# Optimization experiments

Measured on AMD Instinct MI355X. Metric: run time of the kernel, lower is better.

Reference implementation:

```python
import jax, jax.numpy as jnp
import numpy as np

EPS = 1e-8
NUM_ITERATIONS = 3


def layer_norm(x, g, b, eps=EPS):
    m = jnp.mean(x, axis=-1, keepdims=True)
    v = jnp.mean((x - m) ** 2, axis=-1, keepdims=True)
    return (x - m) * jax.lax.rsqrt(v + eps) * g + b


def gru_cell(x, h, w_ih, w_hh, b_ih, b_hh):
    # PyTorch GRUCell: gates ordered (r, z, n)
    gi = x @ w_ih.T + b_ih  # [B*S, 3D]
    gh = h @ w_hh.T + b_hh
    i_r, i_z, i_n = jnp.split(gi, 3, axis=-1)
    h_r, h_z, h_n = jnp.split(gh, 3, axis=-1)
    r = jax.nn.sigmoid(i_r + h_r)
    z = jax.nn.sigmoid(i_z + h_z)
    n = jnp.tanh(i_n + r * h_n)
    return (1.0 - z) * n + z * h


def setup_inputs() -> dict:
    key = jax.random.key(0)
    ks = jax.random.split(key, 12)
    B, N, D, S = 64, 1024, 512, 16
    s = 1.0 / np.sqrt(D)
    return {
        "inputs": jax.random.normal(ks[0], (B, N, D), jnp.float32),
        "noise": jax.random.normal(ks[1], (B, S, D), jnp.float32),
        "slot_mu": jax.random.normal(ks[2], (1, 1, D), jnp.float32),
        "slot_log_sigma": jnp.zeros((1, 1, D), jnp.float32),
        "ln_in_g": jnp.ones((D,), jnp.float32),
        "ln_in_b": jnp.zeros((D,), jnp.float32),
        "ln_slots_g": jnp.ones((D,), jnp.float32),
        "ln_slots_b": jnp.zeros((D,), jnp.float32),
        "ln_mlp_g": jnp.ones((D,), jnp.float32),
        "ln_mlp_b": jnp.zeros((D,), jnp.float32),
        "Wq": jax.random.normal(ks[3], (D, D), jnp.float32) * s,
        "Wk": jax.random.normal(ks[4], (D, D), jnp.float32) * s,
        "Wv": jax.random.normal(ks[5], (D, D), jnp.float32) * s,
        "gru_w_ih": jax.random.normal(ks[6], (3 * D, D), jnp.float32) * s,
        "gru_w_hh": jax.random.normal(ks[7], (3 * D, D), jnp.float32) * s,
        "gru_b_ih": jnp.zeros((3 * D,), jnp.float32),
        "gru_b_hh": jnp.zeros((3 * D,), jnp.float32),
        "mlp_w1": jax.random.normal(ks[8], (D, D), jnp.float32) * s,
        "mlp_b1": jnp.zeros((D,), jnp.float32),
        "mlp_w2": jax.random.normal(ks[9], (D, D), jnp.float32) * s,
        "mlp_b2": jnp.zeros((D,), jnp.float32),
    }


def reference(inputs, noise, slot_mu, slot_log_sigma,
              ln_in_g, ln_in_b, ln_slots_g, ln_slots_b, ln_mlp_g, ln_mlp_b,
              Wq, Wk, Wv, gru_w_ih, gru_w_hh, gru_b_ih, gru_b_hh,
              mlp_w1, mlp_b1, mlp_w2, mlp_b2):
    B, N, D = inputs.shape
    S = noise.shape[1]
    scale = D ** (-0.5)

    # slot init: mu + sigma * eps
    slots = slot_mu + jnp.exp(slot_log_sigma) * noise  # [B,S,D]

    x = layer_norm(inputs, ln_in_g, ln_in_b)
    k = x @ Wk.T  # [B,N,D]
    v = x @ Wv.T

    for _ in range(NUM_ITERATIONS):
        slots_prev = slots
        sn = layer_norm(slots, ln_slots_g, ln_slots_b)
        q = sn @ Wq.T  # [B,S,D]
        attn_logits = jnp.einsum("bnd,bmd->bnm", q, k) * scale  # [B,S,N]
        attn = jax.nn.softmax(attn_logits, axis=-1)
        attn = attn / (jnp.sum(attn, axis=1, keepdims=True) + EPS)  # column-normalize over slots
        updates = jnp.einsum("bnm,bmd->bnd", attn, v)  # [B,S,D]
        slots = gru_cell(updates.reshape(-1, D), slots_prev.reshape(-1, D),
                         gru_w_ih, gru_w_hh, gru_b_ih, gru_b_hh).reshape(B, S, D)
        h = jax.nn.relu(layer_norm(slots, ln_mlp_g, ln_mlp_b) @ mlp_w1.T + mlp_b1)
        slots = slots + h @ mlp_w2.T + mlp_b2

    # proj_to_hidden is Identity (slot_dim == hidden_size); forward_dtype=float32
    return slots
```

## Files before the change

### kernel.cpp

```cpp
#include <hip/hip_runtime.h>
#include <hip/hip_bf16.h>
#include <cstdint>
#include <cstddef>


typedef __bf16 bf16x8 __attribute__((ext_vector_type(8)));
typedef float f32x4 __attribute__((ext_vector_type(4)));

__device__ __forceinline__ float bf2f(unsigned int u) {
  union { unsigned int i; float f; } v; v.i = u << 16; return v.f;
}
__device__ __forceinline__ unsigned short f2bf(float x) {
  __hip_bfloat16 h = __float2bfloat16(x);
  unsigned short u;
  __builtin_memcpy(&u, &h, 2);
  return u;
}

#define GLD16(gp, lp)                                                       \
  __builtin_amdgcn_global_load_lds(                                         \
      (const __attribute__((address_space(1))) void*)(gp),                  \
      (__attribute__((address_space(3))) void*)(lp), 16, 0, 0)


__global__ void cast_bf16_k(const float* __restrict__ in, unsigned short* __restrict__ out, int n) {
  int i = blockIdx.x * 256 + threadIdx.x;
  if (i < n) out[i] = f2bf(in[i]);
}

__global__ __launch_bounds__(256) void tcast_k(const float* __restrict__ in,
                                               unsigned short* __restrict__ out) {
  __shared__ float t[32][33];
  int c0 = blockIdx.x << 5, r0 = blockIdx.y << 5;
  int tx = threadIdx.x & 31, ty = threadIdx.x >> 5;
  #pragma unroll
  for (int i = 0; i < 4; ++i)
    t[ty + 8 * i][tx] = in[(size_t)(r0 + ty + 8 * i) * 512 + c0 + tx];
  __syncthreads();
  #pragma unroll
  for (int i = 0; i < 4; ++i)
    out[(size_t)(c0 + ty + 8 * i) * 512 + r0 + tx] = f2bf(t[tx][ty + 8 * i]);
}

__global__ void init_slots_k(const float* __restrict__ mu, const float* __restrict__ ls,
                             const float* __restrict__ noise, float* __restrict__ slots) {
  int i = blockIdx.x * 256 + threadIdx.x;
  int d = i & 511;
  slots[i] = mu[d] + expf(ls[d]) * noise[i];
}

__global__ void wcat_k(const float* __restrict__ wih, const float* __restrict__ whh,
                       unsigned short* __restrict__ out) {
  int i = blockIdx.x * 256 + threadIdx.x;
  int j = i >> 10, k = i & 1023;
  float v;
  if (j < 1024)      v = (k < 512) ? wih[j * 512 + k] : whh[j * 512 + (k - 512)];
  else if (j < 1536) v = (k < 512) ? wih[j * 512 + k] : 0.0f;
  else               v = (k < 512) ? 0.0f : whh[(j - 512) * 512 + (k - 512)];
  out[i] = f2bf(v);
}

__global__ void bcat_k(const float* __restrict__ bih, const float* __restrict__ bhh,
                       float* __restrict__ out) {
  int j = blockIdx.x * 256 + threadIdx.x;
  float v;
  if (j < 1024)      v = bih[j] + bhh[j];
  else if (j < 1536) v = bih[j];
  else               v = bhh[j - 512];
  out[j] = v;
}


__global__ __launch_bounds__(256) void ln_rows_k(
    const float* __restrict__ in, const float* __restrict__ g, const float* __restrict__ b,
    unsigned short* __restrict__ out, int rows) {
  int w = threadIdx.x >> 6, lane = threadIdx.x & 63;
  int row = (blockIdx.x << 2) + w;
  if (row >= rows) return;
  const float4* rp = reinterpret_cast<const float4*>(in + (size_t)row * 512);
  float4 v0 = rp[lane], v1 = rp[lane + 64];
  float s = v0.x + v0.y + v0.z + v0.w + v1.x + v1.y + v1.z + v1.w;
  float q = v0.x*v0.x + v0.y*v0.y + v0.z*v0.z + v0.w*v0.w
          + v1.x*v1.x + v1.y*v1.y + v1.z*v1.z + v1.w*v1.w;
  #pragma unroll
  for (int o = 32; o > 0; o >>= 1) { s += __shfl_xor(s, o); q += __shfl_xor(q, o); }
  float m = s * (1.0f / 512.0f);
  float rstd = rsqrtf(q * (1.0f / 512.0f) - m * m + 1e-8f);
  const float4* gp = reinterpret_cast<const float4*>(g);
  const float4* bp = reinterpret_cast<const float4*>(b);
  float4 g0 = gp[lane], g1 = gp[lane + 64];
  float4 b0 = bp[lane], b1 = bp[lane + 64];
  ushort4 o0, o1;
  o0.x = f2bf((v0.x - m) * rstd * g0.x + b0.x);
  o0.y = f2bf((v0.y - m) * rstd * g0.y + b0.y);
  o0.z = f2bf((v0.z - m) * rstd * g0.z + b0.z);
  o0.w = f2bf((v0.w - m) * rstd * g0.w + b0.w);
  o1.x = f2bf((v1.x - m) * rstd * g1.x + b1.x);
  o1.y = f2bf((v1.y - m) * rstd * g1.y + b1.y);
  o1.z = f2bf((v1.z - m) * rstd * g1.z + b1.z);
  o1.w = f2bf((v1.w - m) * rstd * g1.w + b1.w);
  ushort4* op = reinterpret_cast<ushort4*>(out + (size_t)row * 512);
  op[lane] = o0; op[lane + 64] = o1;
}

__global__ __launch_bounds__(256) void ln_cast_k(
    const float* __restrict__ in, const float* __restrict__ g, const float* __restrict__ b,
    unsigned short* __restrict__ sn, unsigned short* __restrict__ A2) {
  int w = threadIdx.x >> 6, lane = threadIdx.x & 63;
  int row = (blockIdx.x << 2) + w;
  const float4* rp = reinterpret_cast<const float4*>(in + (size_t)row * 512);
  float4 v0 = rp[lane], v1 = rp[lane + 64];
  float s = v0.x + v0.y + v0.z + v0.w + v1.x + v1.y + v1.z + v1.w;
  float q = v0.x*v0.x + v0.y*v0.y + v0.z*v0.z + v0.w*v0.w
          + v1.x*v1.x + v1.y*v1.y + v1.z*v1.z + v1.w*v1.w;
  #pragma unroll
  for (int o = 32; o > 0; o >>= 1) { s += __shfl_xor(s, o); q += __shfl_xor(q, o); }
  float m = s * (1.0f / 512.0f);
  float rstd = rsqrtf(q * (1.0f / 512.0f) - m * m + 1e-8f);
  const float4* gp = reinterpret_cast<const float4*>(g);
  const float4* bp = reinterpret_cast<const float4*>(b);
  float4 g0 = gp[lane], g1 = gp[lane + 64];
  float4 b0 = bp[lane], b1 = bp[lane + 64];
  ushort4 c0, c1, o0, o1;
  c0.x = f2bf(v0.x); c0.y = f2bf(v0.y); c0.z = f2bf(v0.z); c0.w = f2bf(v0.w);
  c1.x = f2bf(v1.x); c1.y = f2bf(v1.y); c1.z = f2bf(v1.z); c1.w = f2bf(v1.w);
  o0.x = f2bf((v0.x - m) * rstd * g0.x + b0.x);
  o0.y = f2bf((v0.y - m) * rstd * g0.y + b0.y);
  o0.z = f2bf((v0.z - m) * rstd * g0.z + b0.z);
  o0.w = f2bf((v0.w - m) * rstd * g0.w + b0.w);
  o1.x = f2bf((v1.x - m) * rstd * g1.x + b1.x);
  o1.y = f2bf((v1.y - m) * rstd * g1.y + b1.y);
  o1.z = f2bf((v1.z - m) * rstd * g1.z + b1.z);
  o1.w = f2bf((v1.w - m) * rstd * g1.w + b1.w);
  ushort4* sp_ = reinterpret_cast<ushort4*>(sn + (size_t)row * 512);
  ushort4* cp_ = reinterpret_cast<ushort4*>(A2 + (size_t)row * 1024 + 512);
  sp_[lane] = o0; sp_[lane + 64] = o1;
  cp_[lane] = c0; cp_[lane + 64] = c1;
}

__global__ __launch_bounds__(256) void gru_ln_k(
    const float* __restrict__ gates, const float* __restrict__ hp,
    const float* __restrict__ g, const float* __restrict__ b,
    float* __restrict__ sgru, unsigned short* __restrict__ lnm) {
  int w = threadIdx.x >> 6, lane = threadIdx.x & 63;
  int row = (blockIdx.x << 2) + w;
  size_t gb = (size_t)row * 2048 + (lane << 3);
  size_t hb = (size_t)row * 512 + (lane << 3);
  float rs[8], zs[8], in_[8], hn[8], hv[8], y[8];
  #pragma unroll
  for (int c = 0; c < 2; ++c) {
    *reinterpret_cast<float4*>(rs + 4*c)  = *reinterpret_cast<const float4*>(gates + gb + 4*c);
    *reinterpret_cast<float4*>(zs + 4*c)  = *reinterpret_cast<const float4*>(gates + gb + 512 + 4*c);
    *reinterpret_cast<float4*>(in_ + 4*c) = *reinterpret_cast<const float4*>(gates + gb + 1024 + 4*c);
    *reinterpret_cast<float4*>(hn + 4*c)  = *reinterpret_cast<const float4*>(gates + gb + 1536 + 4*c);
    *reinterpret_cast<float4*>(hv + 4*c)  = *reinterpret_cast<const float4*>(hp + hb + 4*c);
  }
  float s = 0.f, q = 0.f;
  #pragma unroll
  for (int j = 0; j < 8; ++j) {
    float r = 1.0f / (1.0f + expf(-rs[j]));
    float z = 1.0f / (1.0f + expf(-zs[j]));
    float n = tanhf(in_[j] + r * hn[j]);
    float h = (1.0f - z) * n + z * hv[j];
    y[j] = h; s += h; q += h * h;
  }
  #pragma unroll
  for (int o = 32; o > 0; o >>= 1) { s += __shfl_xor(s, o); q += __shfl_xor(q, o); }
  float m = s * (1.0f / 512.0f);
  float rstd = rsqrtf(q * (1.0f / 512.0f) - m * m + 1e-8f);
  const float* gg = g + (lane << 3);
  const float* bb = b + (lane << 3);
  #pragma unroll
  for (int c = 0; c < 2; ++c)
    *reinterpret_cast<float4*>(sgru + hb + 4*c) = *reinterpret_cast<const float4*>(y + 4*c);
  uint4 o4;
  unsigned int p[8];
  #pragma unroll
  for (int j = 0; j < 8; ++j) p[j] = f2bf((y[j] - m) * rstd * gg[j] + bb[j]);
  o4.x = p[0] | (p[1] << 16); o4.y = p[2] | (p[3] << 16);
  o4.z = p[4] | (p[5] << 16); o4.w = p[6] | (p[7] << 16);
  *reinterpret_cast<uint4*>(lnm + hb) = o4;
}


__global__ __launch_bounds__(256) void gemm_vt(
    const unsigned short* __restrict__ A, const unsigned short* __restrict__ W,
    unsigned short* __restrict__ vT) {
  __shared__ unsigned short sA[2][4096];
  __shared__ unsigned short sB[2][4096];
  const int tid = threadIdx.x;
  const int lane = tid & 63, w = tid >> 6;

  int flat = blockIdx.y * 4 + blockIdx.x;
  { int c = 2048 >> 3; flat = (flat & 7) * c + (flat >> 3); }
  const int row0 = (flat >> 2) << 7;
  const int col0 = (flat & 3) << 7;
  const int K = 512;

  const int wm = (w >> 1) << 6, wn = (w & 1) << 6;
  const int lrow = lane & 15, kt = (lane >> 4) << 3;
  const int srow = lane >> 2, scol = (lane & 3) << 3;

  f32x4 acc[4][4];
  #pragma unroll
  for (int m = 0; m < 4; ++m)
    #pragma unroll
    for (int n = 0; n < 4; ++n) acc[m][n] = f32x4{0.f, 0.f, 0.f, 0.f};

  auto stage = [&](int buf, int k0) {
    #pragma unroll
    for (int i = 0; i < 2; ++i) {
      int ii = w * 2 + i;
      int r = (ii << 4) + srow;
      GLD16(A + (size_t)(row0 + r) * K + k0 + scol, &sA[buf][ii * 512]);
      GLD16(W + (size_t)(col0 + r) * K + k0 + scol, &sB[buf][ii * 512]);
    }
  };

  stage(0, 0);
  int cur = 0;
  for (int t = 0; t < 16; ++t) {
    __syncthreads();
    if (t + 1 < 16) stage(cur ^ 1, (t + 1) << 5);
    bf16x8 af[4], bfv[4];
    #pragma unroll
    for (int m = 0; m < 4; ++m)
      af[m] = *reinterpret_cast<const bf16x8*>(&sA[cur][(wm + m * 16 + lrow) * 32 + kt]);
    #pragma unroll
    for (int n = 0; n < 4; ++n)
      bfv[n] = *reinterpret_cast<const bf16x8*>(&sB[cur][(wn + n * 16 + lrow) * 32 + kt]);
    #pragma unroll
    for (int m = 0; m < 4; ++m)
      #pragma unroll
      for (int n = 0; n < 4; ++n)
        acc[m][n] = __builtin_amdgcn_mfma_f32_16x16x32_bf16(af[m], bfv[n], acc[m][n], 0, 0, 0);
    cur ^= 1;
  }

  const int rb = (lane >> 4) << 2;
  const int b = row0 >> 10;
  const int n0 = row0 & 1023;
  unsigned short* vb = vT + ((size_t)b << 19);
  #pragma unroll
  for (int m = 0; m < 4; ++m) {
    #pragma unroll
    for (int n = 0; n < 4; ++n) {
      int col = col0 + wn + n * 16 + lrow;
      int nn = n0 + wm + m * 16 + rb;
      ushort4 o;
      o.x = f2bf(acc[m][n][0]); o.y = f2bf(acc[m][n][1]);
      o.z = f2bf(acc[m][n][2]); o.w = f2bf(acc[m][n][3]);
      *reinterpret_cast<ushort4*>(vb + (size_t)col * 1024 + nn) = o;
    }
  }
}


__global__ __launch_bounds__(256) void q2_k(
    const unsigned short* __restrict__ sn, const unsigned short* __restrict__ wpt,
    unsigned short* __restrict__ q2) {
  __shared__ unsigned short sA[2][512];
  __shared__ unsigned short sB[2][4096];
  const int b = blockIdx.y, ct = blockIdx.x;
  const int lane = threadIdx.x & 63, w = threadIdx.x >> 6;
  const int lrow = lane & 15, kt = (lane >> 4) << 3;
  const int srow = lane >> 2, scol = (lane & 3) << 3;
  const unsigned short* Ab = sn + ((size_t)b << 13);
  const unsigned short* Bb = wpt + (size_t)(ct << 7) * 512;

  f32x4 acc[2];
  acc[0] = f32x4{0.f, 0.f, 0.f, 0.f};
  acc[1] = f32x4{0.f, 0.f, 0.f, 0.f};

  auto stage = [&](int buf, int k0) {
    #pragma unroll
    for (int i = 0; i < 2; ++i) {
      int ii = w * 2 + i;
      GLD16(Bb + (size_t)((ii << 4) + srow) * 512 + k0 + scol, &sB[buf][ii * 512]);
    }
    if (w == 0)
      GLD16(Ab + (size_t)srow * 512 + k0 + scol, &sA[buf][0]);
  };

  stage(0, 0);
  int cur = 0;
  for (int t = 0; t < 16; ++t) {
    __syncthreads();
    if (t + 1 < 16) stage(cur ^ 1, (t + 1) << 5);
    bf16x8 af = *reinterpret_cast<const bf16x8*>(&sA[cur][lrow * 32 + kt]);
    #pragma unroll
    for (int ni = 0; ni < 2; ++ni) {
      bf16x8 bfv = *reinterpret_cast<const bf16x8*>(&sB[cur][((w * 2 + ni) * 16 + lrow) * 32 + kt]);
      acc[ni] = __builtin_amdgcn_mfma_f32_16x16x32_bf16(af, bfv, acc[ni], 0, 0, 0);
    }
    cur ^= 1;
  }

  const int rb = (lane >> 4) << 2;
  #pragma unroll
  for (int ni = 0; ni < 2; ++ni) {
    int col = (ct << 7) + (w * 2 + ni) * 16 + lrow;
    #pragma unroll
    for (int r = 0; r < 4; ++r) {
      int s = rb + r;
      q2[(size_t)((b << 4) + s) * 512 + col] = f2bf(acc[ni][r]);
    }
  }
}


__global__ __launch_bounds__(256) void logits_k(
    const unsigned short* __restrict__ q2, const unsigned short* __restrict__ x,
    float* __restrict__ out) {
  __shared__ unsigned short sA[2][512];
  __shared__ unsigned short sB[2][4096];
  const int b = blockIdx.y, nt = blockIdx.x;
  const int lane = threadIdx.x & 63, w = threadIdx.x >> 6;
  const int lrow = lane & 15, kt = (lane >> 4) << 3;
  const int srow = lane >> 2, scol = (lane & 3) << 3;
  const unsigned short* Ab = q2 + ((size_t)b << 13);
  const unsigned short* Bb = x + (((size_t)(b << 10) + (nt << 7)) << 9);

  f32x4 acc[2];
  acc[0] = f32x4{0.f, 0.f, 0.f, 0.f};
  acc[1] = f32x4{0.f, 0.f, 0.f, 0.f};

  auto stage = [&](int buf, int k0) {
    #pragma unroll
    for (int i = 0; i < 2; ++i) {
      int ii = w * 2 + i;
      GLD16(Bb + (size_t)((ii << 4) + srow) * 512 + k0 + scol, &sB[buf][ii * 512]);
    }
    if (w == 0)
      GLD16(Ab + (size_t)srow * 512 + k0 + scol, &sA[buf][0]);
  };

  stage(0, 0);
  int cur = 0;
  for (int t = 0; t < 16; ++t) {
    __syncthreads();
    if (t + 1 < 16) stage(cur ^ 1, (t + 1) << 5);
    bf16x8 af = *reinterpret_cast<const bf16x8*>(&sA[cur][lrow * 32 + kt]);
    #pragma unroll
    for (int ni = 0; ni < 2; ++ni) {
      bf16x8 bfv = *reinterpret_cast<const bf16x8*>(&sB[cur][((w * 2 + ni) * 16 + lrow) * 32 + kt]);
      acc[ni] = __builtin_amdgcn_mfma_f32_16x16x32_bf16(af, bfv, acc[ni], 0, 0, 0);
    }
    cur ^= 1;
  }

  const int rb = (lane >> 4) << 2;
  #pragma unroll
  for (int ni = 0; ni < 2; ++ni) {
    int n = (nt << 7) + (w * 2 + ni) * 16 + lrow;
    #pragma unroll
    for (int r = 0; r < 4; ++r) {
      int s = rb + r;
      out[(size_t)((b << 4) + s) * 1024 + n] = acc[ni][r];
    }
  }
}


__global__ __launch_bounds__(1024) void softmax_cn_k(
    const float* __restrict__ logits, unsigned short* __restrict__ attn) {
  __shared__ float sp[16][1024];
  int b = blockIdx.x;
  int w = threadIdx.x >> 6, lane = threadIdx.x & 63;
  const float* rp = logits + ((size_t)b * 16 + w) * 1024;
  float v[16];
  float mx = -3.4e38f;
  #pragma unroll
  for (int i = 0; i < 16; ++i) { v[i] = rp[lane + (i << 6)]; mx = fmaxf(mx, v[i]); }
  #pragma unroll
  for (int o = 32; o > 0; o >>= 1) mx = fmaxf(mx, __shfl_xor(mx, o));
  float s = 0.f;
  #pragma unroll
  for (int i = 0; i < 16; ++i) { v[i] = __expf(v[i] - mx); s += v[i]; }
  #pragma unroll
  for (int o = 32; o > 0; o >>= 1) s += __shfl_xor(s, o);
  float inv = 1.0f / s;
  #pragma unroll
  for (int i = 0; i < 16; ++i) sp[w][lane + (i << 6)] = v[i] * inv;
  __syncthreads();
  int col = threadIdx.x;
  float cs = 0.f;
  #pragma unroll
  for (int s2 = 0; s2 < 16; ++s2) cs += sp[s2][col];
  float rinv = 1.0f / (cs + 1e-8f);
  unsigned short* ob = attn + ((size_t)b << 14);
  #pragma unroll
  for (int s2 = 0; s2 < 16; ++s2) ob[s2 * 1024 + col] = f2bf(sp[s2][col] * rinv);
}


__global__ __launch_bounds__(256) void pv_k(
    const unsigned short* __restrict__ vT, const unsigned short* __restrict__ attn,
    unsigned short* __restrict__ A2) {
  __shared__ unsigned short sA[2][4096];
  __shared__ unsigned short sB[2][512];
  const int b = blockIdx.y, dt = blockIdx.x;
  const int lane = threadIdx.x & 63, w = threadIdx.x >> 6;
  const int lrow = lane & 15, kt = (lane >> 4) << 3;
  const int srow = lane >> 2, scol = (lane & 3) << 3;
  const unsigned short* Ab = vT + ((size_t)b << 19) + (size_t)(dt << 7) * 1024;
  const unsigned short* Bb = attn + ((size_t)b << 14);

  f32x4 acc[2];
  acc[0] = f32x4{0.f, 0.f, 0.f, 0.f};
  acc[1] = f32x4{0.f, 0.f, 0.f, 0.f};

  auto stage = [&](int buf, int k0) {
    #pragma unroll
    for (int i = 0; i < 2; ++i) {
      int ii = w * 2 + i;
      GLD16(Ab + (size_t)((ii << 4) + srow) * 1024 + k0 + scol, &sA[buf][ii * 512]);
    }
    if (w == 0)
      GLD16(Bb + (size_t)srow * 1024 + k0 + scol, &sB[buf][0]);
  };

  stage(0, 0);
  int cur = 0;
  for (int t = 0; t < 32; ++t) {
    __syncthreads();
    if (t + 1 < 32) stage(cur ^ 1, (t + 1) << 5);
    bf16x8 bfv = *reinterpret_cast<const bf16x8*>(&sB[cur][lrow * 32 + kt]);
    #pragma unroll
    for (int mi = 0; mi < 2; ++mi) {
      bf16x8 af = *reinterpret_cast<const bf16x8*>(&sA[cur][((w * 2 + mi) * 16 + lrow) * 32 + kt]);
      acc[mi] = __builtin_amdgcn_mfma_f32_16x16x32_bf16(af, bfv, acc[mi], 0, 0, 0);
    }
    cur ^= 1;
  }

  const int rb = (lane >> 4) << 2;
  const int s = lrow;
  #pragma unroll
  for (int mi = 0; mi < 2; ++mi) {
    int d0 = (dt << 7) + (w * 2 + mi) * 16 + rb;
    ushort4 o;
    o.x = f2bf(acc[mi][0]); o.y = f2bf(acc[mi][1]);
    o.z = f2bf(acc[mi][2]); o.w = f2bf(acc[mi][3]);
    *reinterpret_cast<ushort4*>(&A2[(size_t)((b << 4) + s) * 1024 + d0]) = o;
  }
}


template<int BIAS, int RELU, int ADDSRC, int OUTBF16, int SCALE>
__global__ __launch_bounds__(256) void gemm_sm(
    const unsigned short* __restrict__ A, const unsigned short* __restrict__ W,
    const float* __restrict__ bias, const float* __restrict__ addsrc,
    void* __restrict__ Cout, int M, int N, int K, float scalev) {
  __shared__ unsigned short sA[2][2048];
  __shared__ unsigned short sB[2][2048];
  const int tid = threadIdx.x;
  const int lane = tid & 63, w = tid >> 6;

  int nwg = gridDim.x * gridDim.y;
  int flat = blockIdx.y * gridDim.x + blockIdx.x;
  if ((nwg & 7) == 0) { int c = nwg >> 3; flat = (flat & 7) * c + (flat >> 3); }
  const int row0 = (flat / gridDim.x) << 6;
  const int col0 = (flat % gridDim.x) << 6;

  const int lrow = lane & 15, kt = (lane >> 4) << 3;
  const int srow = lane >> 2, scol = (lane & 3) << 3;

  f32x4 acc[4];
  #pragma unroll
  for (int m = 0; m < 4; ++m) acc[m] = f32x4{0.f, 0.f, 0.f, 0.f};

  auto stage = [&](int buf, int k0) {
    int r = (w << 4) + srow;
    GLD16(A + (size_t)(row0 + r) * K + k0 + scol, &sA[buf][w * 512]);
    GLD16(W + (size_t)(col0 + r) * K + k0 + scol, &sB[buf][w * 512]);
  };

  stage(0, 0);
  const int nt = K >> 5;
  int cur = 0;
  for (int t = 0; t < nt; ++t) {
    __syncthreads();
    if (t + 1 < nt) stage(cur ^ 1, (t + 1) << 5);
    bf16x8 af[4], bfv;
    #pragma unroll
    for (int m = 0; m < 4; ++m)
      af[m] = *reinterpret_cast<const bf16x8*>(&sA[cur][(m * 16 + lrow) * 32 + kt]);
    bfv = *reinterpret_cast<const bf16x8*>(&sB[cur][((w << 4) + lrow) * 32 + kt]);
    #pragma unroll
    for (int m = 0; m < 4; ++m)
      acc[m] = __builtin_amdgcn_mfma_f32_16x16x32_bf16(af[m], bfv, acc[m], 0, 0, 0);
    cur ^= 1;
  }

  const int rb = (lane >> 4) << 2;
  const int col = col0 + (w << 4) + lrow;
  float bv = BIAS ? bias[col] : 0.0f;
  #pragma unroll
  for (int m = 0; m < 4; ++m) {
    #pragma unroll
    for (int r = 0; r < 4; ++r) {
      int row = row0 + m * 16 + rb + r;
      float v = acc[m][r];
      if (SCALE) v *= scalev;
      v += bv;
      if (ADDSRC) v += addsrc[(size_t)row * N + col];
      if (RELU) v = fmaxf(v, 0.0f);
      if (OUTBF16) ((unsigned short*)Cout)[(size_t)row * N + col] = f2bf(v);
      else ((float*)Cout)[(size_t)row * N + col] = v;
    }
  }
}


extern "C" void kernel_launch(void* const* d_in, const int* in_sizes, int n_in,
                              void* d_out, int out_size, void* d_ws, size_t ws_size,
                              hipStream_t stream) {
  const float* inputs  = (const float*)d_in[0];
  const float* noise   = (const float*)d_in[1];
  const float* slot_mu = (const float*)d_in[2];
  const float* slot_ls = (const float*)d_in[3];
  const float* ln_in_g = (const float*)d_in[4];
  const float* ln_in_b = (const float*)d_in[5];
  const float* ln_s_g  = (const float*)d_in[6];
  const float* ln_s_b  = (const float*)d_in[7];
  const float* ln_m_g  = (const float*)d_in[8];
  const float* ln_m_b  = (const float*)d_in[9];
  const float* Wq   = (const float*)d_in[10];
  const float* Wk   = (const float*)d_in[11];
  const float* Wv   = (const float*)d_in[12];
  const float* w_ih = (const float*)d_in[13];
  const float* w_hh = (const float*)d_in[14];
  const float* b_ih = (const float*)d_in[15];
  const float* b_hh = (const float*)d_in[16];
  const float* w1   = (const float*)d_in[17];
  const float* b1   = (const float*)d_in[18];
  const float* w2   = (const float*)d_in[19];
  const float* b2   = (const float*)d_in[20];

  const int BN = 65536, BS = 1024;

  uintptr_t base = (uintptr_t)d_ws;
  auto alloc = [&](size_t bytes) {
    void* p = (void*)base;
    base += (bytes + 255) & ~(size_t)255;
    return p;
  };
  unsigned short* x_bf    = (unsigned short*)alloc((size_t)BN * 512 * 2);
  unsigned short* vT      = (unsigned short*)alloc((size_t)64 * 512 * 1024 * 2);
  unsigned short* wqT     = (unsigned short*)alloc(512 * 512 * 2);
  unsigned short* wkT     = (unsigned short*)alloc(512 * 512 * 2);
  unsigned short* wpt     = (unsigned short*)alloc(512 * 512 * 2);
  unsigned short* wv_bf   = (unsigned short*)alloc(512 * 512 * 2);
  unsigned short* wcat_bf = (unsigned short*)alloc((size_t)2048 * 1024 * 2);
  float*          bcat    = (float*)alloc(2048 * 4);
  unsigned short* w1_bf   = (unsigned short*)alloc(512 * 512 * 2);
  unsigned short* w2_bf   = (unsigned short*)alloc(512 * 512 * 2);
  float*          slots   = (float*)alloc((size_t)BS * 512 * 4);
  unsigned short* sn_bf   = (unsigned short*)alloc((size_t)BS * 512 * 2);
  unsigned short* A2      = (unsigned short*)alloc((size_t)BS * 1024 * 2);
  unsigned short* q2_bf   = (unsigned short*)alloc((size_t)BS * 512 * 2);
  float*          logits  = (float*)alloc((size_t)64 * 16 * 1024 * 4);
  unsigned short* attn_bf = (unsigned short*)alloc((size_t)64 * 16 * 1024 * 2);
  float*          gates   = (float*)alloc((size_t)BS * 2048 * 4);
  float*          sgru    = (float*)alloc((size_t)BS * 512 * 4);
  unsigned short* lnm_bf  = (unsigned short*)alloc((size_t)BS * 512 * 2);
  unsigned short* h_bf    = (unsigned short*)alloc((size_t)BS * 512 * 2);
  (void)ws_size; (void)n_in; (void)in_sizes; (void)out_size;

  const float scale = 0.044194173824159216f;

  tcast_k<<<dim3(16, 16), 256, 0, stream>>>(Wq, wqT);
  tcast_k<<<dim3(16, 16), 256, 0, stream>>>(Wk, wkT);
  gemm_sm<0,0,0,1,1><<<dim3(8, 8), 256, 0, stream>>>(
      wkT, wqT, nullptr, nullptr, wpt, 512, 512, 512, scale);
  cast_bf16_k<<<1024, 256, 0, stream>>>(Wv, wv_bf, 262144);
  wcat_k<<<8192, 256, 0, stream>>>(w_ih, w_hh, wcat_bf);
  bcat_k<<<8, 256, 0, stream>>>(b_ih, b_hh, bcat);
  cast_bf16_k<<<1024, 256, 0, stream>>>(w1, w1_bf, 262144);
  cast_bf16_k<<<1024, 256, 0, stream>>>(w2, w2_bf, 262144);

  init_slots_k<<<2048, 256, 0, stream>>>(slot_mu, slot_ls, noise, slots);
  ln_rows_k<<<16384, 256, 0, stream>>>(inputs, ln_in_g, ln_in_b, x_bf, BN);
  gemm_vt<<<dim3(4, 512), 256, 0, stream>>>(x_bf, wv_bf, vT);

  for (int it = 0; it < 3; ++it) {
    ln_cast_k<<<256, 256, 0, stream>>>(slots, ln_s_g, ln_s_b, sn_bf, A2);
    q2_k<<<dim3(4, 64), 256, 0, stream>>>(sn_bf, wpt, q2_bf);
    logits_k<<<dim3(8, 64), 256, 0, stream>>>(q2_bf, x_bf, logits);
    softmax_cn_k<<<64, 1024, 0, stream>>>(logits, attn_bf);
    pv_k<<<dim3(4, 64), 256, 0, stream>>>(vT, attn_bf, A2);
    gemm_sm<1,0,0,0,0><<<dim3(32, 16), 256, 0, stream>>>(
        A2, wcat_bf, bcat, nullptr, gates, BS, 2048, 1024, 1.0f);
    gru_ln_k<<<256, 256, 0, stream>>>(gates, slots, ln_m_g, ln_m_b, sgru, lnm_bf);
    gemm_sm<1,1,0,1,0><<<dim3(8, 16), 256, 0, stream>>>(
        lnm_bf, w1_bf, b1, nullptr, h_bf, BS, 512, 512, 1.0f);
    float* slots_out = (it == 2) ? (float*)d_out : slots;
    gemm_sm<1,0,1,0,0><<<dim3(8, 16), 256, 0, stream>>>(
        h_bf, w2_bf, b2, sgru, slots_out, BS, 512, 512, 1.0f);
  }
}
```

Baseline: 365.9 us.

## Fuse slot layernorm into Q GEMM, softmax into PV, and merge setup kernels

Merges the weight cast, concat, bias and slot-init setup kernels into a single launch, and the two transpose-casts into one. In each iteration the slot layernorm moves into the Q-projection kernel and the softmax plus column normalisation moves into the PV kernel, which drops the intermediate sn and attn buffers and several launches. The cost is redundant work: each of the four column tiles recomputes the layernorm and the full softmax for its batch, and extra shared memory is used per block.

Result: no change. 368.9 us (+0.8%).

```diff
diff --git a/kernel.cpp b/kernel.cpp
--- a/kernel.cpp
+++ b/kernel.cpp
@@ -23,51 +23,59 @@
       (__attribute__((address_space(3))) void*)(lp), 16, 0, 0)
 
 
-__global__ void cast_bf16_k(const float* __restrict__ in, unsigned short* __restrict__ out, int n) {
-  int i = blockIdx.x * 256 + threadIdx.x;
-  if (i < n) out[i] = f2bf(in[i]);
-}
-
-__global__ __launch_bounds__(256) void tcast_k(const float* __restrict__ in,
-                                               unsigned short* __restrict__ out) {
-  __shared__ float t[32][33];
+__global__ void wprep_k(const float* __restrict__ Wv, const float* __restrict__ w1,
+                        const float* __restrict__ w2, const float* __restrict__ wih,
+                        const float* __restrict__ whh, const float* __restrict__ bih,
+                        const float* __restrict__ bhh, const float* __restrict__ mu,
+                        const float* __restrict__ ls, const float* __restrict__ noise,
+                        unsigned short* __restrict__ wv_bf, unsigned short* __restrict__ w1_bf,
+                        unsigned short* __restrict__ w2_bf, unsigned short* __restrict__ wcat,
+                        float* __restrict__ bcat, float* __restrict__ slots) {
+  int blk = blockIdx.x, t = threadIdx.x;
+  if (blk < 1024) {
+    int i = blk * 256 + t; wv_bf[i] = f2bf(Wv[i]);
+  } else if (blk < 2048) {
+    int i = (blk - 1024) * 256 + t; w1_bf[i] = f2bf(w1[i]);
+  } else if (blk < 3072) {
+    int i = (blk - 2048) * 256 + t; w2_bf[i] = f2bf(w2[i]);
+  } else if (blk < 11264) {
+    int i = (blk - 3072) * 256 + t;
+    int j = i >> 10, k = i & 1023;
+    float v;
+    if (j < 1024)      v = (k < 512) ? wih[j * 512 + k] : whh[j * 512 + (k - 512)];
+    else if (j < 1536) v = (k < 512) ? wih[j * 512 + k] : 0.0f;
+    else               v = (k < 512) ? 0.0f : whh[(j - 512) * 512 + (k - 512)];
+    wcat[i] = f2bf(v);
+  } else if (blk < 11272) {
+    int j = (blk - 11264) * 256 + t;
+    float v;
+    if (j < 1024)      v = bih[j] + bhh[j];
+    else if (j < 1536) v = bih[j];
+    else               v = bhh[j - 512];
+    bcat[j] = v;
+  } else {
+    int i = (blk - 11272) * 256 + t;
+    int d = i & 511;
+    slots[i] = mu[d] + expf(ls[d]) * noise[i];
+  }
+}
+
+__global__ __launch_bounds__(256) void tcast2_k(const float* __restrict__ Wq,
+                                                const float* __restrict__ Wk,
+                                                unsigned short* __restrict__ wqT,
+                                                unsigned short* __restrict__ wkT) {
+  __shared__ float tt[32][33];
+  const float* in = blockIdx.z ? Wk : Wq;
+  unsigned short* out = blockIdx.z ? wkT : wqT;
   int c0 = blockIdx.x << 5, r0 = blockIdx.y << 5;
   int tx = threadIdx.x & 31, ty = threadIdx.x >> 5;
   #pragma unroll
   for (int i = 0; i < 4; ++i)
-    t[ty + 8 * i][tx] = in[(size_t)(r0 + ty + 8 * i) * 512 + c0 + tx];
+    tt[ty + 8 * i][tx] = in[(size_t)(r0 + ty + 8 * i) * 512 + c0 + tx];
   __syncthreads();
   #pragma unroll
   for (int i = 0; i < 4; ++i)
-    out[(size_t)(c0 + ty + 8 * i) * 512 + r0 + tx] = f2bf(t[tx][ty + 8 * i]);
-}
-
-__global__ void init_slots_k(const float* __restrict__ mu, const float* __restrict__ ls,
-                             const float* __restrict__ noise, float* __restrict__ slots) {
-  int i = blockIdx.x * 256 + threadIdx.x;
-  int d = i & 511;
-  slots[i] = mu[d] + expf(ls[d]) * noise[i];
-}
-
-__global__ void wcat_k(const float* __restrict__ wih, const float* __restrict__ whh,
-                       unsigned short* __restrict__ out) {
-  int i = blockIdx.x * 256 + threadIdx.x;
-  int j = i >> 10, k = i & 1023;
-  float v;
-  if (j < 1024)      v = (k < 512) ? wih[j * 512 + k] : whh[j * 512 + (k - 512)];
-  else if (j < 1536) v = (k < 512) ? wih[j * 512 + k] : 0.0f;
-  else               v = (k < 512) ? 0.0f : whh[(j - 512) * 512 + (k - 512)];
-  out[i] = f2bf(v);
-}
-
-__global__ void bcat_k(const float* __restrict__ bih, const float* __restrict__ bhh,
-                       float* __restrict__ out) {
-  int j = blockIdx.x * 256 + threadIdx.x;
-  float v;
-  if (j < 1024)      v = bih[j] + bhh[j];
-  else if (j < 1536) v = bih[j];
-  else               v = bhh[j - 512];
-  out[j] = v;
+    out[(size_t)(c0 + ty + 8 * i) * 512 + r0 + tx] = f2bf(tt[tx][ty + 8 * i]);
 }
 
 
@@ -103,41 +111,6 @@
   op[lane] = o0; op[lane + 64] = o1;
 }
 
-__global__ __launch_bounds__(256) void ln_cast_k(
-    const float* __restrict__ in, const float* __restrict__ g, const float* __restrict__ b,
-    unsigned short* __restrict__ sn, unsigned short* __restrict__ A2) {
-  int w = threadIdx.x >> 6, lane = threadIdx.x & 63;
-  int row = (blockIdx.x << 2) + w;
-  const float4* rp = reinterpret_cast<const float4*>(in + (size_t)row * 512);
-  float4 v0 = rp[lane], v1 = rp[lane + 64];
-  float s = v0.x + v0.y + v0.z + v0.w + v1.x + v1.y + v1.z + v1.w;
-  float q = v0.x*v0.x + v0.y*v0.y + v0.z*v0.z + v0.w*v0.w
-          + v1.x*v1.x + v1.y*v1.y + v1.z*v1.z + v1.w*v1.w;
-  #pragma unroll
-  for (int o = 32; o > 0; o >>= 1) { s += __shfl_xor(s, o); q += __shfl_xor(q, o); }
-  float m = s * (1.0f / 512.0f);
-  float rstd = rsqrtf(q * (1.0f / 512.0f) - m * m + 1e-8f);
-  const float4* gp = reinterpret_cast<const float4*>(g);
-  const float4* bp = reinterpret_cast<const float4*>(b);
-  float4 g0 = gp[lane], g1 = gp[lane + 64];
-  float4 b0 = bp[lane], b1 = bp[lane + 64];
-  ushort4 c0, c1, o0, o1;
-  c0.x = f2bf(v0.x); c0.y = f2bf(v0.y); c0.z = f2bf(v0.z); c0.w = f2bf(v0.w);
-  c1.x = f2bf(v1.x); c1.y = f2bf(v1.y); c1.z = f2bf(v1.z); c1.w = f2bf(v1.w);
-  o0.x = f2bf((v0.x - m) * rstd * g0.x + b0.x);
-  o0.y = f2bf((v0.y - m) * rstd * g0.y + b0.y);
-  o0.z = f2bf((v0.z - m) * rstd * g0.z + b0.z);
-  o0.w = f2bf((v0.w - m) * rstd * g0.w + b0.w);
-  o1.x = f2bf((v1.x - m) * rstd * g1.x + b1.x);
-  o1.y = f2bf((v1.y - m) * rstd * g1.y + b1.y);
-  o1.z = f2bf((v1.z - m) * rstd * g1.z + b1.z);
-  o1.w = f2bf((v1.w - m) * rstd * g1.w + b1.w);
-  ushort4* sp_ = reinterpret_cast<ushort4*>(sn + (size_t)row * 512);
-  ushort4* cp_ = reinterpret_cast<ushort4*>(A2 + (size_t)row * 1024 + 512);
-  sp_[lane] = o0; sp_[lane + 64] = o1;
-  cp_[lane] = c0; cp_[lane + 64] = c1;
-}
-
 __global__ __launch_bounds__(256) void gru_ln_k(
     const float* __restrict__ gates, const float* __restrict__ hp,
     const float* __restrict__ g, const float* __restrict__ b,
@@ -256,38 +229,73 @@
 }
 
 
-__global__ __launch_bounds__(256) void q2_k(
-    const unsigned short* __restrict__ sn, const unsigned short* __restrict__ wpt,
-    unsigned short* __restrict__ q2) {
-  __shared__ unsigned short sA[2][512];
+__global__ __launch_bounds__(256) void q2ln_k(
+    const float* __restrict__ slots, const float* __restrict__ g, const float* __restrict__ b,
+    const unsigned short* __restrict__ wpt, unsigned short* __restrict__ q2,
+    unsigned short* __restrict__ A2) {
+  __shared__ unsigned short s_sn[16 * 520];
   __shared__ unsigned short sB[2][4096];
-  const int b = blockIdx.y, ct = blockIdx.x;
+  const int b_ = blockIdx.y, ct = blockIdx.x;
   const int lane = threadIdx.x & 63, w = threadIdx.x >> 6;
   const int lrow = lane & 15, kt = (lane >> 4) << 3;
   const int srow = lane >> 2, scol = (lane & 3) << 3;
-  const unsigned short* Ab = sn + ((size_t)b << 13);
+
+  const float4* gp = reinterpret_cast<const float4*>(g);
+  const float4* bp = reinterpret_cast<const float4*>(b);
+  float4 g0 = gp[lane], g1 = gp[lane + 64];
+  float4 b0 = bp[lane], b1 = bp[lane + 64];
+  #pragma unroll
+  for (int rr = 0; rr < 4; ++rr) {
+    int r = w * 4 + rr;
+    const float4* rp = reinterpret_cast<const float4*>(slots + (size_t)(b_ * 16 + r) * 512);
+    float4 v0 = rp[lane], v1 = rp[lane + 64];
+    float s = v0.x + v0.y + v0.z + v0.w + v1.x + v1.y + v1.z + v1.w;
+    float q = v0.x*v0.x + v0.y*v0.y + v0.z*v0.z + v0.w*v0.w
+            + v1.x*v1.x + v1.y*v1.y + v1.z*v1.z + v1.w*v1.w;
+    #pragma unroll
+    for (int o = 32; o > 0; o >>= 1) { s += __shfl_xor(s, o); q += __shfl_xor(q, o); }
+    float m = s * (1.0f / 512.0f);
+    float rstd = rsqrtf(q * (1.0f / 512.0f) - m * m + 1e-8f);
+    ushort4 o0, o1;
+    o0.x = f2bf((v0.x - m) * rstd * g0.x + b0.x);
+    o0.y = f2bf((v0.y - m) * rstd * g0.y + b0.y);
+    o0.z = f2bf((v0.z - m) * rstd * g0.z + b0.z);
+    o0.w = f2bf((v0.w - m) * rstd * g0.w + b0.w);
+    o1.x = f2bf((v1.x - m) * rstd * g1.x + b1.x);
+    o1.y = f2bf((v1.y - m) * rstd * g1.y + b1.y);
+    o1.z = f2bf((v1.z - m) * rstd * g1.z + b1.z);
+    o1.w = f2bf((v1.w - m) * rstd * g1.w + b1.w);
+    *reinterpret_cast<ushort4*>(&s_sn[r * 520 + lane * 4]) = o0;
+    *reinterpret_cast<ushort4*>(&s_sn[r * 520 + 256 + lane * 4]) = o1;
+    if (ct == 0) {
+      ushort4 c0, c1;
+      c0.x = f2bf(v0.x); c0.y = f2bf(v0.y); c0.z = f2bf(v0.z); c0.w = f2bf(v0.w);
+      c1.x = f2bf(v1.x); c1.y = f2bf(v1.y); c1.z = f2bf(v1.z); c1.w = f2bf(v1.w);
+      unsigned short* a2r = A2 + (size_t)(b_ * 16 + r) * 1024 + 512;
+      *reinterpret_cast<ushort4*>(a2r + lane * 4) = c0;
+      *reinterpret_cast<ushort4*>(a2r + 256 + lane * 4) = c1;
+    }
+  }
+
   const unsigned short* Bb = wpt + (size_t)(ct << 7) * 512;
+  auto stage = [&](int buf, int k0) {
+    #pragma unroll
+    for (int i = 0; i < 2; ++i) {
+      int ii = w * 2 + i;
+      GLD16(Bb + (size_t)((ii << 4) + srow) * 512 + k0 + scol, &sB[buf][ii * 512]);
+    }
+  };
 
   f32x4 acc[2];
   acc[0] = f32x4{0.f, 0.f, 0.f, 0.f};
   acc[1] = f32x4{0.f, 0.f, 0.f, 0.f};
-
-  auto stage = [&](int buf, int k0) {
-    #pragma unroll
-    for (int i = 0; i < 2; ++i) {
-      int ii = w * 2 + i;
-      GLD16(Bb + (size_t)((ii << 4) + srow) * 512 + k0 + scol, &sB[buf][ii * 512]);
-    }
-    if (w == 0)
-      GLD16(Ab + (size_t)srow * 512 + k0 + scol, &sA[buf][0]);
-  };
 
   stage(0, 0);
   int cur = 0;
   for (int t = 0; t < 16; ++t) {
     __syncthreads();
     if (t + 1 < 16) stage(cur ^ 1, (t + 1) << 5);
-    bf16x8 af = *reinterpret_cast<const bf16x8*>(&sA[cur][lrow * 32 + kt]);
+    bf16x8 af = *reinterpret_cast<const bf16x8*>(&s_sn[lrow * 520 + (t << 5) + kt]);
     #pragma unroll
     for (int ni = 0; ni < 2; ++ni) {
       bf16x8 bfv = *reinterpret_cast<const bf16x8*>(&sB[cur][((w * 2 + ni) * 16 + lrow) * 32 + kt]);
@@ -303,7 +311,7 @@
     #pragma unroll
     for (int r = 0; r < 4; ++r) {
       int s = rb + r;
-      q2[(size_t)((b << 4) + s) * 512 + col] = f2bf(acc[ni][r]);
+      q2[(size_t)((b_ << 4) + s) * 512 + col] = f2bf(acc[ni][r]);
     }
   }
 }
@@ -362,70 +370,71 @@
 }
 
 
-__global__ __launch_bounds__(1024) void softmax_cn_k(
-    const float* __restrict__ logits, unsigned short* __restrict__ attn) {
-  __shared__ float sp[16][1024];
-  int b = blockIdx.x;
-  int w = threadIdx.x >> 6, lane = threadIdx.x & 63;
-  const float* rp = logits + ((size_t)b * 16 + w) * 1024;
-  float v[16];
-  float mx = -3.4e38f;
-  #pragma unroll
-  for (int i = 0; i < 16; ++i) { v[i] = rp[lane + (i << 6)]; mx = fmaxf(mx, v[i]); }
-  #pragma unroll
-  for (int o = 32; o > 0; o >>= 1) mx = fmaxf(mx, __shfl_xor(mx, o));
-  float s = 0.f;
-  #pragma unroll
-  for (int i = 0; i < 16; ++i) { v[i] = __expf(v[i] - mx); s += v[i]; }
-  #pragma unroll
-  for (int o = 32; o > 0; o >>= 1) s += __shfl_xor(s, o);
-  float inv = 1.0f / s;
-  #pragma unroll
-  for (int i = 0; i < 16; ++i) sp[w][lane + (i << 6)] = v[i] * inv;
-  __syncthreads();
-  int col = threadIdx.x;
-  float cs = 0.f;
-  #pragma unroll
-  for (int s2 = 0; s2 < 16; ++s2) cs += sp[s2][col];
-  float rinv = 1.0f / (cs + 1e-8f);
-  unsigned short* ob = attn + ((size_t)b << 14);
-  #pragma unroll
-  for (int s2 = 0; s2 < 16; ++s2) ob[s2 * 1024 + col] = f2bf(sp[s2][col] * rinv);
-}
-
-
-__global__ __launch_bounds__(256) void pv_k(
-    const unsigned short* __restrict__ vT, const unsigned short* __restrict__ attn,
+__global__ __launch_bounds__(256) void pv_sm_k(
+    const float* __restrict__ logits, const unsigned short* __restrict__ vT,
     unsigned short* __restrict__ A2) {
+  __shared__ float s_mi[16][2];
+  __shared__ unsigned short s_at[16 * 1032];
   __shared__ unsigned short sA[2][4096];
-  __shared__ unsigned short sB[2][512];
-  const int b = blockIdx.y, dt = blockIdx.x;
+  const int b_ = blockIdx.y, dt = blockIdx.x;
   const int lane = threadIdx.x & 63, w = threadIdx.x >> 6;
   const int lrow = lane & 15, kt = (lane >> 4) << 3;
   const int srow = lane >> 2, scol = (lane & 3) << 3;
-  const unsigned short* Ab = vT + ((size_t)b << 19) + (size_t)(dt << 7) * 1024;
-  const unsigned short* Bb = attn + ((size_t)b << 14);
+  const float* lg = logits + ((size_t)b_ << 14);
+
+  #pragma unroll
+  for (int rr = 0; rr < 4; ++rr) {
+    int r = w * 4 + rr;
+    const float* rp = lg + (size_t)r * 1024;
+    float v[16];
+    float mx = -3.4e38f;
+    #pragma unroll
+    for (int i = 0; i < 16; ++i) { v[i] = rp[lane + (i << 6)]; mx = fmaxf(mx, v[i]); }
+    #pragma unroll
+    for (int o = 32; o > 0; o >>= 1) mx = fmaxf(mx, __shfl_xor(mx, o));
+    float s = 0.f;
+    #pragma unroll
+    for (int i = 0; i < 16; ++i) s += __expf(v[i] - mx);
+    #pragma unroll
+    for (int o = 32; o > 0; o >>= 1) s += __shfl_xor(s, o);
+    if (lane == 0) { s_mi[r][0] = mx; s_mi[r][1] = 1.0f / s; }
+  }
+  __syncthreads();
+
+  #pragma unroll
+  for (int j = 0; j < 4; ++j) {
+    int c = threadIdx.x + (j << 8);
+    float e[16];
+    float cs = 0.f;
+    #pragma unroll
+    for (int s = 0; s < 16; ++s) {
+      e[s] = __expf(lg[(size_t)s * 1024 + c] - s_mi[s][0]) * s_mi[s][1];
+      cs += e[s];
+    }
+    float rv = 1.0f / (cs + 1e-8f);
+    #pragma unroll
+    for (int s = 0; s < 16; ++s) s_at[s * 1032 + c] = f2bf(e[s] * rv);
+  }
+
+  const unsigned short* Ab = vT + ((size_t)b_ << 19) + (size_t)(dt << 7) * 1024;
+  auto stage = [&](int buf, int k0) {
+    #pragma unroll
+    for (int i = 0; i < 2; ++i) {
+      int ii = w * 2 + i;
+      GLD16(Ab + (size_t)((ii << 4) + srow) * 1024 + k0 + scol, &sA[buf][ii * 512]);
+    }
+  };
 
   f32x4 acc[2];
   acc[0] = f32x4{0.f, 0.f, 0.f, 0.f};
   acc[1] = f32x4{0.f, 0.f, 0.f, 0.f};
-
-  auto stage = [&](int buf, int k0) {
-    #pragma unroll
-    for (int i = 0; i < 2; ++i) {
-      int ii = w * 2 + i;
-      GLD16(Ab + (size_t)((ii << 4) + srow) * 1024 + k0 + scol, &sA[buf][ii * 512]);
-    }
-    if (w == 0)
-      GLD16(Bb + (size_t)srow * 1024 + k0 + scol, &sB[buf][0]);
-  };
 
   stage(0, 0);
   int cur = 0;
   for (int t = 0; t < 32; ++t) {
     __syncthreads();
     if (t + 1 < 32) stage(cur ^ 1, (t + 1) << 5);
-    bf16x8 bfv = *reinterpret_cast<const bf16x8*>(&sB[cur][lrow * 32 + kt]);
+    bf16x8 bfv = *reinterpret_cast<const bf16x8*>(&s_at[lrow * 1032 + (t << 5) + kt]);
     #pragma unroll
     for (int mi = 0; mi < 2; ++mi) {
       bf16x8 af = *reinterpret_cast<const bf16x8*>(&sA[cur][((w * 2 + mi) * 16 + lrow) * 32 + kt]);
@@ -442,7 +451,7 @@
     ushort4 o;
     o.x = f2bf(acc[mi][0]); o.y = f2bf(acc[mi][1]);
     o.z = f2bf(acc[mi][2]); o.w = f2bf(acc[mi][3]);
-    *reinterpret_cast<ushort4*>(&A2[(size_t)((b << 4) + s) * 1024 + d0]) = o;
+    *reinterpret_cast<ushort4*>(&A2[(size_t)((b_ << 4) + s) * 1024 + d0]) = o;
   }
 }
 
@@ -557,11 +566,9 @@
   unsigned short* w1_bf   = (unsigned short*)alloc(512 * 512 * 2);
   unsigned short* w2_bf   = (unsigned short*)alloc(512 * 512 * 2);
   float*          slots   = (float*)alloc((size_t)BS * 512 * 4);
-  unsigned short* sn_bf   = (unsigned short*)alloc((size_t)BS * 512 * 2);
   unsigned short* A2      = (unsigned short*)alloc((size_t)BS * 1024 * 2);
   unsigned short* q2_bf   = (unsigned short*)alloc((size_t)BS * 512 * 2);
   float*          logits  = (float*)alloc((size_t)64 * 16 * 1024 * 4);
-  unsigned short* attn_bf = (unsigned short*)alloc((size_t)64 * 16 * 1024 * 2);
   float*          gates   = (float*)alloc((size_t)BS * 2048 * 4);
   float*          sgru    = (float*)alloc((size_t)BS * 512 * 4);
   unsigned short* lnm_bf  = (unsigned short*)alloc((size_t)BS * 512 * 2);
@@ -570,26 +577,19 @@
 
   const float scale = 0.044194173824159216f;
 
-  tcast_k<<<dim3(16, 16), 256, 0, stream>>>(Wq, wqT);
-  tcast_k<<<dim3(16, 16), 256, 0, stream>>>(Wk, wkT);
+  wprep_k<<<13320, 256, 0, stream>>>(Wv, w1, w2, w_ih, w_hh, b_ih, b_hh,
+                                     slot_mu, slot_ls, noise,
+                                     wv_bf, w1_bf, w2_bf, wcat_bf, bcat, slots);
+  tcast2_k<<<dim3(16, 16, 2), 256, 0, stream>>>(Wq, Wk, wqT, wkT);
   gemm_sm<0,0,0,1,1><<<dim3(8, 8), 256, 0, stream>>>(
       wkT, wqT, nullptr, nullptr, wpt, 512, 512, 512, scale);
-  cast_bf16_k<<<1024, 256, 0, stream>>>(Wv, wv_bf, 262144);
-  wcat_k<<<8192, 256, 0, stream>>>(w_ih, w_hh, wcat_bf);
-  bcat_k<<<8, 256, 0, stream>>>(b_ih, b_hh, bcat);
-  cast_bf16_k<<<1024, 256, 0, stream>>>(w1, w1_bf, 262144);
-  cast_bf16_k<<<1024, 256, 0, stream>>>(w2, w2_bf, 262144);
-
-  init_slots_k<<<2048, 256, 0, stream>>>(slot_mu, slot_ls, noise, slots);
   ln_rows_k<<<16384, 256, 0, stream>>>(inputs, ln_in_g, ln_in_b, x_bf, BN);
   gemm_vt<<<dim3(4, 512), 256, 0, stream>>>(x_bf, wv_bf, vT);
 
   for (int it = 0; it < 3; ++it) {
-    ln_cast_k<<<256, 256, 0, stream>>>(slots, ln_s_g, ln_s_b, sn_bf, A2);
-    q2_k<<<dim3(4, 64), 256, 0, stream>>>(sn_bf, wpt, q2_bf);
+    q2ln_k<<<dim3(4, 64), 256, 0, stream>>>(slots, ln_s_g, ln_s_b, wpt, q2_bf, A2);
     logits_k<<<dim3(8, 64), 256, 0, stream>>>(q2_bf, x_bf, logits);
-    softmax_cn_k<<<64, 1024, 0, stream>>>(logits, attn_bf);
-    pv_k<<<dim3(4, 64), 256, 0, stream>>>(vT, attn_bf, A2);
+    pv_sm_k<<<dim3(4, 64), 256, 0, stream>>>(logits, vT, A2);
     gemm_sm<1,0,0,0,0><<<dim3(32, 16), 256, 0, stream>>>(
         A2, wcat_bf, bcat, nullptr, gates, BS, 2048, 1024, 1.0f);
     gru_ln_k<<<256, 256, 0, stream>>>(gates, slots, ln_m_g, ln_m_b, sgru, lnm_bf);
```
